# Kernel optimization log

Hardware: AMD Instinct MI355X
Metric: run time of the kernel (lower is better)

The kernel has to match this reference:

```python
import jax, jax.numpy as jnp
import numpy as np

B = 16384      # batch
IN = 512       # input width
G, F, O = 64, 24, 16      # hidden: groups, fan_in, group_out (width = G*O = 1024)
GO_G, GO_F, GO_O = 4, 48, 16  # output layer: 4 groups x 16 = 64 outputs


def setup_inputs() -> dict:
    key = jax.random.key(0)
    ks = jax.random.split(key, 13)
    # total columns available (concat of input + all prior hidden layers)
    tot = [IN, IN + G * O, IN + 2 * G * O, IN + 3 * G * O]  # 512,1536,2560,3584
    scale = 0.1
    return {
        "x": jax.random.normal(ks[0], (B, IN), jnp.float32),
        "W1": jax.random.normal(ks[1], (G, F, O), jnp.float32) * scale,
        "b1": jnp.zeros((G, O), jnp.float32),
        "W2": jax.random.normal(ks[2], (G, F, O), jnp.float32) * scale,
        "b2": jnp.zeros((G, O), jnp.float32),
        "W3": jax.random.normal(ks[3], (G, F, O), jnp.float32) * scale,
        "b3": jnp.zeros((G, O), jnp.float32),
        "Wo": jax.random.normal(ks[4], (GO_G, GO_F, GO_O), jnp.float32) * scale,
        "bo": jnp.zeros((GO_G, GO_O), jnp.float32),
        "idx1": jax.random.randint(ks[5], (G, F), 0, tot[0], jnp.int32),
        "idx2": jax.random.randint(ks[6], (G, F), 0, tot[1], jnp.int32),
        "idx3": jax.random.randint(ks[7], (G, F), 0, tot[2], jnp.int32),
        "idxo": jax.random.randint(ks[8], (GO_G, GO_F), 0, tot[3], jnp.int32),
    }


def _group_layer(acc, idx, W, b, act):
    # acc: [B, P] concat of all prior layer outputs; idx: [G, F] column coords
    g = acc[:, idx]                               # [B, G, F] irregular gather
    h = jnp.einsum('bgf,gfo->bgo', g, W) + b      # many tiny dense sublayers
    h = act(h)
    return h.reshape(h.shape[0], -1)              # concat groups -> [B, G*O]


def reference(x, W1, b1, W2, b2, W3, b3, Wo, bo, idx1, idx2, idx3, idxo):
    acc = x
    for idx, W, b in ((idx1, W1, b1), (idx2, W2, b2), (idx3, W3, b3)):
        out = _group_layer(acc, idx, W, b, jnp.tanh)
        acc = jnp.concatenate([acc, out], axis=1)  # inputs.append(layer_out)
    # output layer uses linear out_activation
    return _group_layer(acc, idxo, Wo, bo, lambda h: h)  # [B, 64]
```

## Files before the change

### kernel.cpp

```cpp
#include <hip/hip_runtime.h>
#include <hip/hip_bf16.h>


typedef unsigned short ushort_t;
typedef unsigned int uint_t;
typedef __attribute__((ext_vector_type(8))) short short8;
typedef __attribute__((ext_vector_type(4))) float f32x4;

#define ACC_STRIDE 3588
#define ROW_BYTES (ACC_STRIDE * 2)
#define PAD_ONE 3584
#define ONE_BYTE (PAD_ONE * 2)
#define ZERO_BYTE (3586 * 2)
#define ACC_U16 (16 * ACC_STRIDE)
#define LDS_BYTES (ACC_U16 * 2)

#define OFF_HID_B 204800
#define OFF_HEAD_B 229376

__device__ __forceinline__ ushort_t f2bf(float f) {
    __hip_bfloat16 h = __float2bfloat16(f);
    union { __hip_bfloat16 h; ushort_t u; } v;
    v.h = h;
    return v.u;
}

__device__ __forceinline__ uint_t pack2bf(float lo, float hi) {
    return (uint_t)f2bf(lo) | ((uint_t)f2bf(hi) << 16);
}

__device__ __forceinline__ float fast_tanh(float x) {
    float e = __expf(2.0f * x);
    return fmaf(-2.0f, __builtin_amdgcn_rcpf(e + 1.0f), 1.0f);
}

__global__ __launch_bounds__(256)
void convert_weights(const float* __restrict__ W1, const float* __restrict__ b1,
                     const float* __restrict__ W2, const float* __restrict__ b2,
                     const float* __restrict__ W3, const float* __restrict__ b3,
                     const float* __restrict__ Wo, const float* __restrict__ bo,
                     const int* __restrict__ idx1, const int* __restrict__ idx2,
                     const int* __restrict__ idx3, const int* __restrict__ idxo,
                     ushort_t* __restrict__ ws)
{
    const int tid = blockIdx.x * 256 + threadIdx.x;
    const int lane = tid & 63;
    const int nn = lane & 15;
    const int quad = lane >> 4;
    if (tid < 12288) {
        const int g = (tid >> 6) & 63;
        const int l = tid >> 12;
        const float* W = (l == 0) ? W1 : (l == 1) ? W2 : W3;
        const float* bb = (l == 0) ? b1 : (l == 1) ? b2 : b3;
        const float* Wg = W + g * 384;
        ushort_t v[8];
        #pragma unroll
        for (int j = 0; j < 8; ++j) {
            const int k = quad * 8 + j;
            v[j] = (k < 24) ? f2bf(Wg[k * 16 + nn])
                 : (k == 24) ? f2bf(bb[g * 16 + nn]) : (ushort_t)0;
        }
        ushort4* dst = reinterpret_cast<ushort4*>(ws + (size_t)tid * 8);
        dst[0] = make_ushort4(v[0], v[1], v[2], v[3]);
        dst[1] = make_ushort4(v[4], v[5], v[6], v[7]);
    } else if (tid < 12800) {
        const int h = tid - 12288;
        const int gs = h >> 6;
        const int go = gs >> 1;
        const int step = gs & 1;
        const float* Wg = Wo + go * 768;
        ushort_t v[8];
        #pragma unroll
        for (int j = 0; j < 8; ++j) {
            const int k = step * 32 + quad * 8 + j;
            v[j] = (k < 48) ? f2bf(Wg[k * 16 + nn])
                 : (k == 48) ? f2bf(bo[go * 16 + nn]) : (ushort_t)0;
        }
        ushort4* dst = reinterpret_cast<ushort4*>(ws + (size_t)tid * 8);
        dst[0] = make_ushort4(v[0], v[1], v[2], v[3]);
        dst[1] = make_ushort4(v[4], v[5], v[6], v[7]);
    } else if (tid < 18944) {
        const int e = tid - 12800;
        const int l = e >> 11;
        const int rem = e & 2047;
        const int g = rem >> 5;
        const int k = rem & 31;
        const int* idx = (l == 0) ? idx1 : (l == 1) ? idx2 : idx3;
        const int v = (k < 24) ? idx[g * 24 + k] * 2
                    : (k == 24) ? ONE_BYTE : ZERO_BYTE;
        reinterpret_cast<int*>((char*)ws + OFF_HID_B)[e] = v;
    } else if (tid < 19200) {
        const int e = tid - 18944;
        const int go = e >> 6;
        const int k = e & 63;
        const int v = (k < 48) ? idxo[go * 48 + k] * 2
                    : (k == 48) ? ONE_BYTE : ZERO_BYTE;
        reinterpret_cast<int*>((char*)ws + OFF_HEAD_B)[e] = v;
    }
}

#define NTILES 4

__global__ __launch_bounds__(1024)
void demodel_mfma(const float* __restrict__ x,
                  const ushort_t* __restrict__ ws,
                  float* __restrict__ out)
{
    extern __shared__ __align__(16) ushort_t smem[];
    const int t = threadIdx.x;
    const int lane = t & 63;
    const int wv = t >> 6;
    const int nn = lane & 15;
    const int quad = lane >> 4;

    const int* offs = reinterpret_cast<const int*>((const char*)ws + OFF_HID_B);

    if (t < 16) {
        uint2* p = reinterpret_cast<uint2*>((char*)smem + t * ROW_BYTES + ONE_BYTE);
        *p = make_uint2(0x00003f80u, 0u);
    }

    const char* accb = (const char*)smem + nn * ROW_BYTES;
    char* accw = (char*)smem;

    const int pr = (t - 512) >> 5;
    const int pc = (t & 31) << 4;
    uint_t px[8];

    if (wv >= 8) {
        const float4* src = reinterpret_cast<const float4*>(
            x + ((size_t)blockIdx.x * 16 + pr) * 512 + pc);
        float4 a0 = src[0], a1 = src[1], a2 = src[2], a3 = src[3];
        px[0] = pack2bf(a0.x, a0.y); px[1] = pack2bf(a0.z, a0.w);
        px[2] = pack2bf(a1.x, a1.y); px[3] = pack2bf(a1.z, a1.w);
        px[4] = pack2bf(a2.x, a2.y); px[5] = pack2bf(a2.z, a2.w);
        px[6] = pack2bf(a3.x, a3.y); px[7] = pack2bf(a3.z, a3.w);
    }

    #pragma unroll 1
    for (int it = 0; it < NTILES; ++it) {
        const int row0 = (it * 256 + blockIdx.x) * 16;

        __syncthreads();
        if (wv >= 8) {
            uint2* d = reinterpret_cast<uint2*>(accw + pr * ROW_BYTES + pc * 2);
            d[0] = make_uint2(px[0], px[1]);
            d[1] = make_uint2(px[2], px[3]);
            d[2] = make_uint2(px[4], px[5]);
            d[3] = make_uint2(px[6], px[7]);
        }
        __syncthreads();

        #pragma unroll 1
        for (int l = 0; l < 3; ++l) {
            const int out_base = 512 + l * 1024;
            const int g0 = wv << 2;

            int4 o0[4], o1[4];
            short8 bfr[4];
            #pragma unroll
            for (int gi = 0; gi < 4; ++gi) {
                const int* op = offs + l * 2048 + (g0 + gi) * 32 + quad * 8;
                o0[gi] = *reinterpret_cast<const int4*>(op);
                o1[gi] = *reinterpret_cast<const int4*>(op + 4);
                bfr[gi] = *reinterpret_cast<const short8*>(
                    ws + (((size_t)l * 64 + g0 + gi) * 64 + lane) * 8);
            }

            short8 af[4];
            #pragma unroll
            for (int gi = 0; gi < 4; ++gi) {
                af[gi][0] = *(const short*)(accb + o0[gi].x);
                af[gi][1] = *(const short*)(accb + o0[gi].y);
                af[gi][2] = *(const short*)(accb + o0[gi].z);
                af[gi][3] = *(const short*)(accb + o0[gi].w);
                af[gi][4] = *(const short*)(accb + o1[gi].x);
                af[gi][5] = *(const short*)(accb + o1[gi].y);
                af[gi][6] = *(const short*)(accb + o1[gi].z);
                af[gi][7] = *(const short*)(accb + o1[gi].w);
            }

            f32x4 acc[4];
            #pragma unroll
            for (int gi = 0; gi < 4; ++gi) {
                f32x4 z = { 0.f, 0.f, 0.f, 0.f };
                acc[gi] = __builtin_amdgcn_mfma_f32_16x16x32_bf16(bfr[gi], af[gi], z, 0, 0, 0);
            }

            #pragma unroll
            for (int gi = 0; gi < 4; ++gi) {
                const int colo = out_base + (g0 + gi) * 16 + quad * 4;
                uint2 w = make_uint2(
                    pack2bf(fast_tanh(acc[gi][0]), fast_tanh(acc[gi][1])),
                    pack2bf(fast_tanh(acc[gi][2]), fast_tanh(acc[gi][3])));
                *reinterpret_cast<uint2*>(accw + nn * ROW_BYTES + colo * 2) = w;
            }
            __syncthreads();
        }

        if (wv < 4) {
            const int go = wv;
            int4 o0[2], o1[2];
            short8 bfr[2];
            #pragma unroll
            for (int s = 0; s < 2; ++s) {
                const int* op = offs + 6144 + go * 64 + s * 32 + quad * 8;
                o0[s] = *reinterpret_cast<const int4*>(op);
                o1[s] = *reinterpret_cast<const int4*>(op + 4);
                bfr[s] = *reinterpret_cast<const short8*>(
                    ws + (12288 + ((size_t)go * 2 + s) * 64 + lane) * 8);
            }
            short8 af[2];
            #pragma unroll
            for (int s = 0; s < 2; ++s) {
                af[s][0] = *(const short*)(accb + o0[s].x);
                af[s][1] = *(const short*)(accb + o0[s].y);
                af[s][2] = *(const short*)(accb + o0[s].z);
                af[s][3] = *(const short*)(accb + o0[s].w);
                af[s][4] = *(const short*)(accb + o1[s].x);
                af[s][5] = *(const short*)(accb + o1[s].y);
                af[s][6] = *(const short*)(accb + o1[s].z);
                af[s][7] = *(const short*)(accb + o1[s].w);
            }
            f32x4 z = { 0.f, 0.f, 0.f, 0.f };
            f32x4 a0 = __builtin_amdgcn_mfma_f32_16x16x32_bf16(bfr[0], af[0], z, 0, 0, 0);
            f32x4 a1 = __builtin_amdgcn_mfma_f32_16x16x32_bf16(bfr[1], af[1], z, 0, 0, 0);
            float4 o;
            o.x = a0[0] + a1[0];
            o.y = a0[1] + a1[1];
            o.z = a0[2] + a1[2];
            o.w = a0[3] + a1[3];
            *reinterpret_cast<float4*>(
                out + (size_t)(row0 + nn) * 64 + go * 16 + quad * 4) = o;
        }
        if (wv >= 8 && it + 1 < NTILES) {
            const float4* src = reinterpret_cast<const float4*>(
                x + (((size_t)(it + 1) * 256 + blockIdx.x) * 16 + pr) * 512 + pc);
            float4 a0 = src[0], a1 = src[1], a2 = src[2], a3 = src[3];
            px[0] = pack2bf(a0.x, a0.y); px[1] = pack2bf(a0.z, a0.w);
            px[2] = pack2bf(a1.x, a1.y); px[3] = pack2bf(a1.z, a1.w);
            px[4] = pack2bf(a2.x, a2.y); px[5] = pack2bf(a2.z, a2.w);
            px[6] = pack2bf(a3.x, a3.y); px[7] = pack2bf(a3.z, a3.w);
        }
    }
}

extern "C" void kernel_launch(void* const* d_in, const int* in_sizes, int n_in,
                              void* d_out, int out_size, void* d_ws, size_t ws_size,
                              hipStream_t stream) {
    const float* x  = (const float*)d_in[0];
    const float* W1 = (const float*)d_in[1];
    const float* b1 = (const float*)d_in[2];
    const float* W2 = (const float*)d_in[3];
    const float* b2 = (const float*)d_in[4];
    const float* W3 = (const float*)d_in[5];
    const float* b3 = (const float*)d_in[6];
    const float* Wo = (const float*)d_in[7];
    const float* bo = (const float*)d_in[8];
    const int* idx1 = (const int*)d_in[9];
    const int* idx2 = (const int*)d_in[10];
    const int* idx3 = (const int*)d_in[11];
    const int* idxo = (const int*)d_in[12];
    float* out = (float*)d_out;

    (void)hipFuncSetAttribute((const void*)demodel_mfma,
                              hipFuncAttributeMaxDynamicSharedMemorySize,
                              LDS_BYTES);

    convert_weights<<<75, 256, 0, stream>>>(W1, b1, W2, b2, W3, b3, Wo, bo,
                                            idx1, idx2, idx3, idxo,
                                            (ushort_t*)d_ws);

    demodel_mfma<<<256, 1024, LDS_BYTES, stream>>>(
        x, (const ushort_t*)d_ws, out);
}
```

Baseline: 128.2 us.

## Fuse weight conversion into main kernel with register-resident weights and LDS offsets

Removes the separate convert_weights launch. Each block now builds the gather offset table in LDS and converts its own bf16 weight fragments into registers once, keeping them across all tiles. Each layer is split into two half-layers separated by a sched_barrier. This removes a kernel launch, the global workspace round-trip, and the per-layer global weight and offset loads. In exchange every block redundantly reads and converts the fp32 weights, and holding 14 short8 fragments in registers adds register pressure at 1024 threads per block.

```diff
diff --git a/kernel.cpp b/kernel.cpp
--- a/kernel.cpp
+++ b/kernel.cpp
@@ -13,10 +13,8 @@
 #define ONE_BYTE (PAD_ONE * 2)
 #define ZERO_BYTE (3586 * 2)
 #define ACC_U16 (16 * ACC_STRIDE)
-#define LDS_BYTES (ACC_U16 * 2)
-
-#define OFF_HID_B 204800
-#define OFF_HEAD_B 229376
+#define OFFS_INTS 6400
+#define LDS_BYTES (ACC_U16 * 2 + OFFS_INTS * 4)
 
 __device__ __forceinline__ ushort_t f2bf(float f) {
     __hip_bfloat16 h = __float2bfloat16(f);
@@ -34,76 +32,16 @@
     return fmaf(-2.0f, __builtin_amdgcn_rcpf(e + 1.0f), 1.0f);
 }
 
-__global__ __launch_bounds__(256)
-void convert_weights(const float* __restrict__ W1, const float* __restrict__ b1,
-                     const float* __restrict__ W2, const float* __restrict__ b2,
-                     const float* __restrict__ W3, const float* __restrict__ b3,
-                     const float* __restrict__ Wo, const float* __restrict__ bo,
-                     const int* __restrict__ idx1, const int* __restrict__ idx2,
-                     const int* __restrict__ idx3, const int* __restrict__ idxo,
-                     ushort_t* __restrict__ ws)
-{
-    const int tid = blockIdx.x * 256 + threadIdx.x;
-    const int lane = tid & 63;
-    const int nn = lane & 15;
-    const int quad = lane >> 4;
-    if (tid < 12288) {
-        const int g = (tid >> 6) & 63;
-        const int l = tid >> 12;
-        const float* W = (l == 0) ? W1 : (l == 1) ? W2 : W3;
-        const float* bb = (l == 0) ? b1 : (l == 1) ? b2 : b3;
-        const float* Wg = W + g * 384;
-        ushort_t v[8];
-        #pragma unroll
-        for (int j = 0; j < 8; ++j) {
-            const int k = quad * 8 + j;
-            v[j] = (k < 24) ? f2bf(Wg[k * 16 + nn])
-                 : (k == 24) ? f2bf(bb[g * 16 + nn]) : (ushort_t)0;
-        }
-        ushort4* dst = reinterpret_cast<ushort4*>(ws + (size_t)tid * 8);
-        dst[0] = make_ushort4(v[0], v[1], v[2], v[3]);
-        dst[1] = make_ushort4(v[4], v[5], v[6], v[7]);
-    } else if (tid < 12800) {
-        const int h = tid - 12288;
-        const int gs = h >> 6;
-        const int go = gs >> 1;
-        const int step = gs & 1;
-        const float* Wg = Wo + go * 768;
-        ushort_t v[8];
-        #pragma unroll
-        for (int j = 0; j < 8; ++j) {
-            const int k = step * 32 + quad * 8 + j;
-            v[j] = (k < 48) ? f2bf(Wg[k * 16 + nn])
-                 : (k == 48) ? f2bf(bo[go * 16 + nn]) : (ushort_t)0;
-        }
-        ushort4* dst = reinterpret_cast<ushort4*>(ws + (size_t)tid * 8);
-        dst[0] = make_ushort4(v[0], v[1], v[2], v[3]);
-        dst[1] = make_ushort4(v[4], v[5], v[6], v[7]);
-    } else if (tid < 18944) {
-        const int e = tid - 12800;
-        const int l = e >> 11;
-        const int rem = e & 2047;
-        const int g = rem >> 5;
-        const int k = rem & 31;
-        const int* idx = (l == 0) ? idx1 : (l == 1) ? idx2 : idx3;
-        const int v = (k < 24) ? idx[g * 24 + k] * 2
-                    : (k == 24) ? ONE_BYTE : ZERO_BYTE;
-        reinterpret_cast<int*>((char*)ws + OFF_HID_B)[e] = v;
-    } else if (tid < 19200) {
-        const int e = tid - 18944;
-        const int go = e >> 6;
-        const int k = e & 63;
-        const int v = (k < 48) ? idxo[go * 48 + k] * 2
-                    : (k == 48) ? ONE_BYTE : ZERO_BYTE;
-        reinterpret_cast<int*>((char*)ws + OFF_HEAD_B)[e] = v;
-    }
-}
-
 #define NTILES 4
 
 __global__ __launch_bounds__(1024)
 void demodel_mfma(const float* __restrict__ x,
-                  const ushort_t* __restrict__ ws,
+                  const float* __restrict__ W1, const float* __restrict__ b1,
+                  const float* __restrict__ W2, const float* __restrict__ b2,
+                  const float* __restrict__ W3, const float* __restrict__ b3,
+                  const float* __restrict__ Wo, const float* __restrict__ bo,
+                  const int* __restrict__ idx1, const int* __restrict__ idx2,
+                  const int* __restrict__ idx3, const int* __restrict__ idxo,
                   float* __restrict__ out)
 {
     extern __shared__ __align__(16) ushort_t smem[];
@@ -113,16 +51,6 @@
     const int nn = lane & 15;
     const int quad = lane >> 4;
 
-    const int* offs = reinterpret_cast<const int*>((const char*)ws + OFF_HID_B);
-
-    if (t < 16) {
-        uint2* p = reinterpret_cast<uint2*>((char*)smem + t * ROW_BYTES + ONE_BYTE);
-        *p = make_uint2(0x00003f80u, 0u);
-    }
-
-    const char* accb = (const char*)smem + nn * ROW_BYTES;
-    char* accw = (char*)smem;
-
     const int pr = (t - 512) >> 5;
     const int pc = (t & 31) << 4;
     uint_t px[8];
@@ -137,6 +65,124 @@
         px[6] = pack2bf(a3.x, a3.y); px[7] = pack2bf(a3.z, a3.w);
     }
 
+    int* offs_w = reinterpret_cast<int*>(smem + ACC_U16);
+    for (int e = t; e < OFFS_INTS; e += 1024) {
+        int v;
+        if (e < 6144) {
+            const int l = e >> 11;
+            const int rem = e & 2047;
+            const int g = rem >> 5;
+            const int k = rem & 31;
+            const int* idx = (l == 0) ? idx1 : (l == 1) ? idx2 : idx3;
+            v = (k < 24) ? idx[g * 24 + k] * 2
+              : (k == 24) ? ONE_BYTE : ZERO_BYTE;
+        } else {
+            const int e2 = e - 6144;
+            const int go = e2 >> 6;
+            const int k = e2 & 63;
+            v = (k < 48) ? idxo[go * 48 + k] * 2
+              : (k == 48) ? ONE_BYTE : ZERO_BYTE;
+        }
+        offs_w[e] = v;
+    }
+
+    if (t < 16) {
+        uint2* p = reinterpret_cast<uint2*>((char*)smem + t * ROW_BYTES + ONE_BYTE);
+        *p = make_uint2(0x00003f80u, 0u);
+    }
+
+    short8 wfr[12];
+    #pragma unroll
+    for (int l = 0; l < 3; ++l) {
+        const float* W = (l == 0) ? W1 : (l == 1) ? W2 : W3;
+        const float* bb = (l == 0) ? b1 : (l == 1) ? b2 : b3;
+        #pragma unroll
+        for (int u = 0; u < 4; ++u) {
+            const int g = (wv << 2) + u;
+            short8 v;
+            if (quad < 3) {
+                const float* p = W + g * 384 + (quad * 8) * 16 + nn;
+                #pragma unroll
+                for (int j = 0; j < 8; ++j) v[j] = (short)f2bf(p[j * 16]);
+            } else {
+                #pragma unroll
+                for (int j = 0; j < 8; ++j) v[j] = 0;
+                v[0] = (short)f2bf(bb[g * 16 + nn]);
+            }
+            wfr[l * 4 + u] = v;
+        }
+    }
+    short8 hwf[2];
+    if (wv < 4) {
+        #pragma unroll
+        for (int s = 0; s < 2; ++s) {
+            const int k0 = s * 32 + quad * 8;
+            short8 v;
+            if (k0 < 48) {
+                const float* p = Wo + wv * 768 + k0 * 16 + nn;
+                #pragma unroll
+                for (int j = 0; j < 8; ++j) v[j] = (short)f2bf(p[j * 16]);
+            } else if (k0 == 48) {
+                #pragma unroll
+                for (int j = 0; j < 8; ++j) v[j] = 0;
+                v[0] = (short)f2bf(bo[wv * 16 + nn]);
+            } else {
+                #pragma unroll
+                for (int j = 0; j < 8; ++j) v[j] = 0;
+            }
+            hwf[s] = v;
+        }
+    }
+
+    const int* offs = offs_w;
+    const char* accb = (const char*)smem + nn * ROW_BYTES;
+    char* accw = (char*)smem;
+
+#define HALF_LAYER(L, HB)                                                   \
+    {                                                                       \
+        const int g0 = (wv << 2) + ((HB) << 1);                             \
+        int4 o0[2], o1[2];                                                  \
+        _Pragma("unroll")                                                   \
+        for (int gi = 0; gi < 2; ++gi) {                                    \
+            const int* op = offs + (L) * 2048 + (g0 + gi) * 32 + quad * 8;  \
+            o0[gi] = *reinterpret_cast<const int4*>(op);                    \
+            o1[gi] = *reinterpret_cast<const int4*>(op + 4);                \
+        }                                                                   \
+        short8 af[2];                                                       \
+        _Pragma("unroll")                                                   \
+        for (int gi = 0; gi < 2; ++gi) {                                    \
+            af[gi][0] = *(const short*)(accb + o0[gi].x);                   \
+            af[gi][1] = *(const short*)(accb + o0[gi].y);                   \
+            af[gi][2] = *(const short*)(accb + o0[gi].z);                   \
+            af[gi][3] = *(const short*)(accb + o0[gi].w);                   \
+            af[gi][4] = *(const short*)(accb + o1[gi].x);                   \
+            af[gi][5] = *(const short*)(accb + o1[gi].y);                   \
+            af[gi][6] = *(const short*)(accb + o1[gi].z);                   \
+            af[gi][7] = *(const short*)(accb + o1[gi].w);                   \
+        }                                                                   \
+        f32x4 acc[2];                                                       \
+        _Pragma("unroll")                                                   \
+        for (int gi = 0; gi < 2; ++gi) {                                    \
+            f32x4 z = { 0.f, 0.f, 0.f, 0.f };                               \
+            acc[gi] = __builtin_amdgcn_mfma_f32_16x16x32_bf16(              \
+                wfr[(L) * 4 + (HB) * 2 + gi], af[gi], z, 0, 0, 0);          \
+        }                                                                   \
+        _Pragma("unroll")                                                   \
+        for (int gi = 0; gi < 2; ++gi) {                                    \
+            const int colo = 512 + (L) * 1024 + (g0 + gi) * 16 + quad * 4;  \
+            uint2 w = make_uint2(                                           \
+                pack2bf(fast_tanh(acc[gi][0]), fast_tanh(acc[gi][1])),      \
+                pack2bf(fast_tanh(acc[gi][2]), fast_tanh(acc[gi][3])));     \
+            *reinterpret_cast<uint2*>(accw + nn * ROW_BYTES + colo * 2) = w;\
+        }                                                                   \
+    }
+
+#define LAYER(L)                                                            \
+    HALF_LAYER(L, 0)                                                        \
+    __builtin_amdgcn_sched_barrier(0);                                      \
+    HALF_LAYER(L, 1)                                                        \
+    __syncthreads();
+
     #pragma unroll 1
     for (int it = 0; it < NTILES; ++it) {
         const int row0 = (it * 256 + blockIdx.x) * 16;
@@ -151,64 +197,18 @@
         }
         __syncthreads();
 
-        #pragma unroll 1
-        for (int l = 0; l < 3; ++l) {
-            const int out_base = 512 + l * 1024;
-            const int g0 = wv << 2;
-
-            int4 o0[4], o1[4];
-            short8 bfr[4];
-            #pragma unroll
-            for (int gi = 0; gi < 4; ++gi) {
-                const int* op = offs + l * 2048 + (g0 + gi) * 32 + quad * 8;
-                o0[gi] = *reinterpret_cast<const int4*>(op);
-                o1[gi] = *reinterpret_cast<const int4*>(op + 4);
-                bfr[gi] = *reinterpret_cast<const short8*>(
-                    ws + (((size_t)l * 64 + g0 + gi) * 64 + lane) * 8);
-            }
-
-            short8 af[4];
-            #pragma unroll
-            for (int gi = 0; gi < 4; ++gi) {
-                af[gi][0] = *(const short*)(accb + o0[gi].x);
-                af[gi][1] = *(const short*)(accb + o0[gi].y);
-                af[gi][2] = *(const short*)(accb + o0[gi].z);
-                af[gi][3] = *(const short*)(accb + o0[gi].w);
-                af[gi][4] = *(const short*)(accb + o1[gi].x);
-                af[gi][5] = *(const short*)(accb + o1[gi].y);
-                af[gi][6] = *(const short*)(accb + o1[gi].z);
-                af[gi][7] = *(const short*)(accb + o1[gi].w);
-            }
-
-            f32x4 acc[4];
-            #pragma unroll
-            for (int gi = 0; gi < 4; ++gi) {
-                f32x4 z = { 0.f, 0.f, 0.f, 0.f };
-                acc[gi] = __builtin_amdgcn_mfma_f32_16x16x32_bf16(bfr[gi], af[gi], z, 0, 0, 0);
-            }
-
-            #pragma unroll
-            for (int gi = 0; gi < 4; ++gi) {
-                const int colo = out_base + (g0 + gi) * 16 + quad * 4;
-                uint2 w = make_uint2(
-                    pack2bf(fast_tanh(acc[gi][0]), fast_tanh(acc[gi][1])),
-                    pack2bf(fast_tanh(acc[gi][2]), fast_tanh(acc[gi][3])));
-                *reinterpret_cast<uint2*>(accw + nn * ROW_BYTES + colo * 2) = w;
-            }
-            __syncthreads();
-        }
+        LAYER(0)
+        LAYER(1)
+        LAYER(2)
 
         if (wv < 4) {
             const int go = wv;
             int4 o0[2], o1[2];
-            short8 bfr[2];
             #pragma unroll
             for (int s = 0; s < 2; ++s) {
                 const int* op = offs + 6144 + go * 64 + s * 32 + quad * 8;
                 o0[s] = *reinterpret_cast<const int4*>(op);
                 o1[s] = *reinterpret_cast<const int4*>(op + 4);
-                bfr[s] = *reinterpret_cast<const short8*>(
-                    ws + (12288 + ((size_t)go * 2 + s) * 64 + lane) * 8);
             }
             short8 af[2];
             #pragma unroll
@@ -223,8 +223,8 @@
                 af[s][7] = *(const short*)(accb + o1[s].w);
             }
             f32x4 z = { 0.f, 0.f, 0.f, 0.f };
-            f32x4 a0 = __builtin_amdgcn_mfma_f32_16x16x32_bf16(bfr[0], af[0], z, 0, 0, 0);
-            f32x4 a1 = __builtin_amdgcn_mfma_f32_16x16x32_bf16(bfr[1], af[1], z, 0, 0, 0);
+            f32x4 a0 = __builtin_amdgcn_mfma_f32_16x16x32_bf16(hwf[0], af[0], z, 0, 0, 0);
+            f32x4 a1 = __builtin_amdgcn_mfma_f32_16x16x32_bf16(hwf[1], af[1], z, 0, 0, 0);
             float4 o;
             o.x = a0[0] + a1[0];
             o.y = a0[1] + a1[1];
@@ -243,6 +243,8 @@
             px[6] = pack2bf(a3.x, a3.y); px[7] = pack2bf(a3.z, a3.w);
         }
     }
+#undef LAYER
+#undef HALF_LAYER
 }
 
 extern "C" void kernel_launch(void* const* d_in, const int* in_sizes, int n_in,
@@ -262,15 +264,12 @@
     const int* idx3 = (const int*)d_in[11];
     const int* idxo = (const int*)d_in[12];
     float* out = (float*)d_out;
+    (void)d_ws; (void)ws_size;
 
     (void)hipFuncSetAttribute((const void*)demodel_mfma,
                               hipFuncAttributeMaxDynamicSharedMemorySize,
                               LDS_BYTES);
 
-    convert_weights<<<75, 256, 0, stream>>>(W1, b1, W2, b2, W3, b3, Wo, bo,
-                                            idx1, idx2, idx3, idxo,
-                                            (ushort_t*)d_ws);
-
     demodel_mfma<<<256, 1024, LDS_BYTES, stream>>>(
-        x, (const ushort_t*)d_ws, out);
-}
+        x, W1, b1, W2, b2, W3, b3, Wo, bo, idx1, idx2, idx3, idxo, out);
+}
```

Result: no change. 127.1 us (-0.9%).
